# Kernel tuning notes

Hardware: AMD Instinct MI355X
Metric: run time of the kernel (lower is better)

The kernel has to match this reference:

```python
import jax, jax.numpy as jnp
import numpy as np

NEG_INF = -9e15  # matches torch reference mask value
LEAKY_SLOPE = 0.2  # alpha passed to nn.LeakyReLU


def setup_inputs() -> dict:
    key = jax.random.key(0)
    k1, k2, k3 = jax.random.split(key, 3)
    B, N, E = 256, 300, 100
    item_embeddings = jax.random.normal(k1, (B, N, E), dtype=jnp.float32)
    adj = jax.random.randint(k2, (B, N, N), 0, 5, dtype=jnp.int64)  # edge types 0..4
    A = jax.random.normal(k3, (4, E), dtype=jnp.float32)  # stacked a_0..a_3
    return {"item_embeddings": item_embeddings, "adj": adj, "A": A}


def reference(item_embeddings, adj, A):
    h = item_embeddings  # [B, N, E]
    # Original: a_input[b,i,j,:] = h[b,i,:] * h[b,j,:]; e_k = leakyrelu(a_input @ a_k).
    # Equivalent without the (B,N,N,E) tensor: e_k[b,i,j] = lrelu(sum_d h[b,i,d] h[b,j,d] A[k,d]).
    e = jnp.einsum('bid,bjd,kd->kbij', h, h, A)  # [4, B, N, N]
    e = jax.nn.leaky_relu(e, LEAKY_SLOPE)
    mask = jnp.full_like(e[0], NEG_INF)
    alpha = jnp.where(adj == 1, e[0], mask)
    alpha = jnp.where(adj == 2, e[1], alpha)
    alpha = jnp.where(adj == 3, e[2], alpha)
    alpha = jnp.where(adj == 4, e[3], alpha)
    alpha = jax.nn.softmax(alpha, axis=-1)
    return jnp.matmul(alpha, h)  # [B, N, E]
```

## Files before the change

kernel.cpp:

```cpp
#include <hip/hip_runtime.h>


typedef _Float16 half8 __attribute__((ext_vector_type(8)));
typedef _Float16 half4 __attribute__((ext_vector_type(4)));
typedef float f32x4 __attribute__((ext_vector_type(4)));

constexpr int B_ = 256, N_ = 300, E_ = 100;
constexpr float NEGINF = -9e15f;
constexpr float PADV   = -3e38f;
constexpr float LOG2E  = 1.44269504088896f;

constexpr int PART_OFF  = 69120;
constexpr int LDS_BYTES = 69120 + 11 * 7680;

#define TRD(dst, addr, off) \
  asm volatile("ds_read_b64_tr_b16 %0, %1 offset:" #off : "=v"(dst) : "v"(addr))
#define LGKM0 do { asm volatile("s_waitcnt lgkmcnt(0)" ::: "memory"); \
                   __builtin_amdgcn_sched_barrier(0); } while (0)

__global__ __launch_bounds__(768)
void gat_flash16(const float* __restrict__ H, const int* __restrict__ ADJ,
                 const float* __restrict__ A, float* __restrict__ OUT) {
  extern __shared__ char smraw[];
  _Float16* hS   = (_Float16*)smraw;
  _Float16* A16  = (_Float16*)(smraw + 68096);
  float*    part = (float*)(smraw + PART_OFF);

  const int b = blockIdx.x;
  const int tid = threadIdx.x;
  const int w = tid >> 6, lane = tid & 63;
  const int lg = lane >> 4, ll = lane & 15;

  const float* Hb  = H + (size_t)b * (N_ * E_);
  const int*   AJb = ADJ + (size_t)b * (N_ * N_);

  for (int u = tid; u < 304 * 14; u += 768) {
    const int j = u / 14, hr = u % 14;
    half8 v;
#pragma unroll
    for (int e = 0; e < 8; ++e) {
      const int d = hr * 8 + e;
      v[e] = (_Float16)((j < N_ && d < E_) ? Hb[j * E_ + d] : 0.f);
    }
    *(half8*)&hS[(((j >> 4) * 7 + (hr >> 1)) << 8) + ((j & 15) << 4) + ((hr & 1) << 3)] = v;
  }
  if (tid < 64) {
    const int k = tid >> 4, oct = tid & 15;
    half8 v;
#pragma unroll
    for (int e = 0; e < 8; ++e) {
      const int d = oct * 8 + e;
      v[e] = (_Float16)((d < E_) ? A[k * E_ + d] * LOG2E : 0.f);
    }
    *(half8*)&A16[k * 128 + oct * 8] = v;
  }
  __syncthreads();

  const unsigned ldsbase = (unsigned)(size_t)(void*)hS;
  const unsigned trlane  = (unsigned)(ll * 8 + lg * 128);

  half8 g[3][4];
  half4 gt[4];
  float m, lsum;
  f32x4 acc[7];
  const int* ajrow = AJb;

  auto prep_strip = [&](int s) {
    const int irow = s * 16 + ll;
    const int irc  = irow < N_ ? irow : N_ - 1;
    ajrow = AJb + (size_t)irc * N_;
#pragma unroll
    for (int db = 0; db < 3; ++db) {
      const int doct = db * 4 + lg;
      const half8 hi = *(const half8*)&hS[((s * 7 + (doct >> 1)) << 8) + (ll << 4) + ((doct & 1) << 3)];
#pragma unroll
      for (int k = 0; k < 4; ++k)
        g[db][k] = hi * *(const half8*)&A16[k * 128 + doct * 8];
    }
    const half4 hit = *(const half4*)&hS[((s * 7 + 6) << 8) + (ll << 4) + lg * 4];
#pragma unroll
    for (int k = 0; k < 4; ++k)
      gt[k] = hit * *(const half4*)&A16[k * 128 + 96 + lg * 4];
    m = PADV; lsum = 0.f;
#pragma unroll
    for (int t = 0; t < 7; ++t) acc[t] = (f32x4){0.f, 0.f, 0.f, 0.f};
  };

  auto load_adj = [&](int jt) -> int4 {
    int jc = jt * 16 + lg * 4;
    if (jc > N_ - 4) jc = N_ - 4;
    return *(const int4*)(ajrow + jc);
  };

  auto tile_body = [&](int jt, int4 av, bool tail) {
    f32x4 c0 = {0.f, 0.f, 0.f, 0.f}, c1 = c0, c2 = c0, c3 = c0;
#pragma unroll
    for (int db = 0; db < 3; ++db) {
      const int doct = db * 4 + lg;
      const half8 aj = *(const half8*)&hS[((jt * 7 + (doct >> 1)) << 8) + (ll << 4) + ((doct & 1) << 3)];
      c0 = __builtin_amdgcn_mfma_f32_16x16x32_f16(aj, g[db][0], c0, 0, 0, 0);
      c1 = __builtin_amdgcn_mfma_f32_16x16x32_f16(aj, g[db][1], c1, 0, 0, 0);
      c2 = __builtin_amdgcn_mfma_f32_16x16x32_f16(aj, g[db][2], c2, 0, 0, 0);
      c3 = __builtin_amdgcn_mfma_f32_16x16x32_f16(aj, g[db][3], c3, 0, 0, 0);
    }
    {
      const half4 ajt = *(const half4*)&hS[((jt * 7 + 6) << 8) + (ll << 4) + lg * 4];
      c0 = __builtin_amdgcn_mfma_f32_16x16x16f16(ajt, gt[0], c0, 0, 0, 0);
      c1 = __builtin_amdgcn_mfma_f32_16x16x16f16(ajt, gt[1], c1, 0, 0, 0);
      c2 = __builtin_amdgcn_mfma_f32_16x16x16f16(ajt, gt[2], c2, 0, 0, 0);
      c3 = __builtin_amdgcn_mfma_f32_16x16x16f16(ajt, gt[3], c3, 0, 0, 0);
    }
    const int va[4] = {av.x, av.y, av.z, av.w};
    float sv[4];
#pragma unroll
    for (int r = 0; r < 4; ++r) {
      const float e = (va[r] == 1) ? c0[r] : (va[r] == 2) ? c1[r]
                     : (va[r] == 3) ? c2[r] : c3[r];
      sv[r] = (va[r] == 0) ? NEGINF : fmaxf(e, 0.2f * e);
    }
    if (tail && lg == 3) { sv[0] = PADV; sv[1] = PADV; sv[2] = PADV; sv[3] = PADV; }

    const unsigned trb = ldsbase + (unsigned)(jt * 3584) + trlane;
    half4 tr[7];
    TRD(tr[0], trb, 0);    TRD(tr[1], trb, 512);  TRD(tr[2], trb, 1024);
    TRD(tr[3], trb, 1536); TRD(tr[4], trb, 2048); TRD(tr[5], trb, 2560);
    TRD(tr[6], trb, 3072);

    const float lmax = fmaxf(fmaxf(sv[0], sv[1]), fmaxf(sv[2], sv[3]));
    if (__any(lmax > m + 8.f)) {
      float tmax = fmaxf(lmax, __shfl_xor(lmax, 16));
      tmax = fmaxf(tmax, __shfl_xor(tmax, 32));
      const float nm = fmaxf(m, tmax);
      const float f = exp2f(m - nm);
      m = nm; lsum *= f;
#pragma unroll
      for (int t = 0; t < 7; ++t) {
        acc[t][0] *= f; acc[t][1] *= f; acc[t][2] *= f; acc[t][3] *= f;
      }
    }
    const float p0 = exp2f(sv[0] - m), p1 = exp2f(sv[1] - m);
    const float p2 = exp2f(sv[2] - m), p3 = exp2f(sv[3] - m);
    lsum += (p0 + p1) + (p2 + p3);
    half4 pb;
    pb[0] = (_Float16)p0; pb[1] = (_Float16)p1;
    pb[2] = (_Float16)p2; pb[3] = (_Float16)p3;

    LGKM0;
#pragma unroll
    for (int t = 0; t < 7; ++t)
      acc[t] = __builtin_amdgcn_mfma_f32_16x16x16f16(tr[t], pb, acc[t], 0, 0, 0);
  };

  auto store_rows = [&](int s) {
    float ls = lsum;
    ls += __shfl_xor(ls, 16);
    ls += __shfl_xor(ls, 32);
    const float rv = 1.f / ls;
    const int irow = s * 16 + ll;
    if (irow < N_) {
      float* orow = OUT + ((size_t)b * N_ + irow) * E_;
#pragma unroll
      for (int t = 0; t < 7; ++t) {
        const int e0 = t * 16 + lg * 4;
        if (e0 < E_) {
          f32x4 o = acc[t];
          o[0] *= rv; o[1] *= rv; o[2] *= rv; o[3] *= rv;
          *(f32x4*)&orow[e0] = o;
        }
      }
    }
  };

  int u = 30 * w;
  const int u1 = (w == 11) ? 361 : (u + 30);
  bool held = false;
  int s_held = 0;

  while (u < u1) {
    const int s  = u / 19;
    const int j0 = u - 19 * s;
    const int j1 = (19 < j0 + (u1 - u)) ? 19 : (j0 + (u1 - u));
    prep_strip(s);
    int4 av = load_adj(j0);
    for (int jt = j0; jt < j1; ++jt) {
      const int4 nv = (jt + 1 < j1) ? load_adj(jt + 1) : av;
      tile_body(jt, av, jt == 18);
      av = nv;
    }
    if (j0 > 0) {
      float* dst = part + (size_t)(w - 1) * 1920 + lane * 30;
#pragma unroll
      for (int t = 0; t < 7; ++t) {
        dst[4 * t + 0] = acc[t][0]; dst[4 * t + 1] = acc[t][1];
        dst[4 * t + 2] = acc[t][2]; dst[4 * t + 3] = acc[t][3];
      }
      dst[28] = m; dst[29] = lsum;
    } else if (j1 < 19) {
      held = true; s_held = s;
    } else {
      store_rows(s);
    }
    u += j1 - j0;
  }

  __syncthreads();

  if (held) {
    const float* src = part + (size_t)w * 1920 + lane * 30;
    const float mq = src[28], lq = src[29];
    const float M  = fmaxf(m, mq);
    const float f0 = exp2f(m - M), f1 = exp2f(mq - M);
    m = M;
    lsum = lsum * f0 + lq * f1;
#pragma unroll
    for (int t = 0; t < 7; ++t) {
      acc[t][0] = acc[t][0] * f0 + src[4 * t + 0] * f1;
      acc[t][1] = acc[t][1] * f0 + src[4 * t + 1] * f1;
      acc[t][2] = acc[t][2] * f0 + src[4 * t + 2] * f1;
      acc[t][3] = acc[t][3] * f0 + src[4 * t + 3] * f1;
    }
    store_rows(s_held);
  }
}

extern "C" void kernel_launch(void* const* d_in, const int* in_sizes, int n_in,
                              void* d_out, int out_size, void* d_ws, size_t ws_size,
                              hipStream_t stream) {
  const float* H  = (const float*)d_in[0];
  const int*   AJ = (const int*)d_in[1];
  const float* A  = (const float*)d_in[2];
  float* OUT = (float*)d_out;

  (void)hipFuncSetAttribute(reinterpret_cast<const void*>(gat_flash16),
                            hipFuncAttributeMaxDynamicSharedMemorySize,
                            LDS_BYTES);
  gat_flash16<<<B_, 768, LDS_BYTES, stream>>>(H, AJ, A, OUT);
}
```

Baseline: 67.73 us.

## Process key tiles in pairs per online-softmax step and rebalance wave work units

```diff
diff --git a/kernel.cpp b/kernel.cpp
--- a/kernel.cpp
+++ b/kernel.cpp
@@ -19,7 +19,7 @@
                    __builtin_amdgcn_sched_barrier(0); } while (0)
 
 __global__ __launch_bounds__(768)
-void gat_flash16(const float* __restrict__ H, const int* __restrict__ ADJ,
+void gat_flash17(const float* __restrict__ H, const int* __restrict__ ADJ,
                  const float* __restrict__ A, float* __restrict__ OUT) {
   extern __shared__ char smraw[];
   _Float16* hS   = (_Float16*)smraw;
@@ -90,6 +90,100 @@
     int jc = jt * 16 + lg * 4;
     if (jc > N_ - 4) jc = N_ - 4;
     return *(const int4*)(ajrow + jc);
+  };
+
+  auto pair_body = [&](int jtA, int4 av0, int4 av1) {
+    f32x4 c0 = {0.f, 0.f, 0.f, 0.f}, c1 = c0, c2 = c0, c3 = c0;
+#pragma unroll
+    for (int db = 0; db < 3; ++db) {
+      const int doct = db * 4 + lg;
+      const half8 aj = *(const half8*)&hS[((jtA * 7 + (doct >> 1)) << 8) + (ll << 4) + ((doct & 1) << 3)];
+      c0 = __builtin_amdgcn_mfma_f32_16x16x32_f16(aj, g[db][0], c0, 0, 0, 0);
+      c1 = __builtin_amdgcn_mfma_f32_16x16x32_f16(aj, g[db][1], c1, 0, 0, 0);
+      c2 = __builtin_amdgcn_mfma_f32_16x16x32_f16(aj, g[db][2], c2, 0, 0, 0);
+      c3 = __builtin_amdgcn_mfma_f32_16x16x32_f16(aj, g[db][3], c3, 0, 0, 0);
+    }
+    {
+      const half4 ajt = *(const half4*)&hS[((jtA * 7 + 6) << 8) + (ll << 4) + lg * 4];
+      c0 = __builtin_amdgcn_mfma_f32_16x16x16f16(ajt, gt[0], c0, 0, 0, 0);
+      c1 = __builtin_amdgcn_mfma_f32_16x16x16f16(ajt, gt[1], c1, 0, 0, 0);
+      c2 = __builtin_amdgcn_mfma_f32_16x16x16f16(ajt, gt[2], c2, 0, 0, 0);
+      c3 = __builtin_amdgcn_mfma_f32_16x16x16f16(ajt, gt[3], c3, 0, 0, 0);
+    }
+    const int vaA[4] = {av0.x, av0.y, av0.z, av0.w};
+    float svA[4];
+#pragma unroll
+    for (int r = 0; r < 4; ++r) {
+      const float e = (vaA[r] == 1) ? c0[r] : (vaA[r] == 2) ? c1[r]
+                     : (vaA[r] == 3) ? c2[r] : c3[r];
+      svA[r] = (vaA[r] == 0) ? NEGINF : fmaxf(e, 0.2f * e);
+    }
+    const int jtB = jtA + 1;
+    f32x4 d0 = {0.f, 0.f, 0.f, 0.f}, d1 = d0, d2 = d0, d3 = d0;
+#pragma unroll
+    for (int db = 0; db < 3; ++db) {
+      const int doct = db * 4 + lg;
+      const half8 aj = *(const half8*)&hS[((jtB * 7 + (doct >> 1)) << 8) + (ll << 4) + ((doct & 1) << 3)];
+      d0 = __builtin_amdgcn_mfma_f32_16x16x32_f16(aj, g[db][0], d0, 0, 0, 0);
+      d1 = __builtin_amdgcn_mfma_f32_16x16x32_f16(aj, g[db][1], d1, 0, 0, 0);
+      d2 = __builtin_amdgcn_mfma_f32_16x16x32_f16(aj, g[db][2], d2, 0, 0, 0);
+      d3 = __builtin_amdgcn_mfma_f32_16x16x32_f16(aj, g[db][3], d3, 0, 0, 0);
+    }
+    {
+      const half4 ajt = *(const half4*)&hS[((jtB * 7 + 6) << 8) + (ll << 4) + lg * 4];
+      d0 = __builtin_amdgcn_mfma_f32_16x16x16f16(ajt, gt[0], d0, 0, 0, 0);
+      d1 = __builtin_amdgcn_mfma_f32_16x16x16f16(ajt, gt[1], d1, 0, 0, 0);
+      d2 = __builtin_amdgcn_mfma_f32_16x16x16f16(ajt, gt[2], d2, 0, 0, 0);
+      d3 = __builtin_amdgcn_mfma_f32_16x16x16f16(ajt, gt[3], d3, 0, 0, 0);
+    }
+    const int vaB[4] = {av1.x, av1.y, av1.z, av1.w};
+    float svB[4];
+#pragma unroll
+    for (int r = 0; r < 4; ++r) {
+      const float e = (vaB[r] == 1) ? d0[r] : (vaB[r] == 2) ? d1[r]
+                     : (vaB[r] == 3) ? d2[r] : d3[r];
+      svB[r] = (vaB[r] == 0) ? NEGINF : fmaxf(e, 0.2f * e);
+    }
+
+    const unsigned trbA = ldsbase + (unsigned)(jtA * 3584) + trlane;
+    half4 hfA[7], hfB[7];
+    TRD(hfA[0], trbA, 0);    TRD(hfA[1], trbA, 512);  TRD(hfA[2], trbA, 1024);
+    TRD(hfA[3], trbA, 1536); TRD(hfA[4], trbA, 2048); TRD(hfA[5], trbA, 2560);
+    TRD(hfA[6], trbA, 3072);
+    TRD(hfB[0], trbA, 3584); TRD(hfB[1], trbA, 4096); TRD(hfB[2], trbA, 4608);
+    TRD(hfB[3], trbA, 5120); TRD(hfB[4], trbA, 5632); TRD(hfB[5], trbA, 6144);
+    TRD(hfB[6], trbA, 6656);
+
+    const float lmax = fmaxf(fmaxf(fmaxf(svA[0], svA[1]), fmaxf(svA[2], svA[3])),
+                             fmaxf(fmaxf(svB[0], svB[1]), fmaxf(svB[2], svB[3])));
+    if (__any(lmax > m + 8.f)) {
+      float tmax = fmaxf(lmax, __shfl_xor(lmax, 16));
+      tmax = fmaxf(tmax, __shfl_xor(tmax, 32));
+      const float nm = fmaxf(m, tmax);
+      const float f = exp2f(m - nm);
+      m = nm; lsum *= f;
+#pragma unroll
+      for (int t = 0; t < 7; ++t) {
+        acc[t][0] *= f; acc[t][1] *= f; acc[t][2] *= f; acc[t][3] *= f;
+      }
+    }
+    const float pA0 = exp2f(svA[0] - m), pA1 = exp2f(svA[1] - m);
+    const float pA2 = exp2f(svA[2] - m), pA3 = exp2f(svA[3] - m);
+    const float pB0 = exp2f(svB[0] - m), pB1 = exp2f(svB[1] - m);
+    const float pB2 = exp2f(svB[2] - m), pB3 = exp2f(svB[3] - m);
+    lsum += ((pA0 + pA1) + (pA2 + pA3)) + ((pB0 + pB1) + (pB2 + pB3));
+    half4 pbA, pbB;
+    pbA[0] = (_Float16)pA0; pbA[1] = (_Float16)pA1;
+    pbA[2] = (_Float16)pA2; pbA[3] = (_Float16)pA3;
+    pbB[0] = (_Float16)pB0; pbB[1] = (_Float16)pB1;
+    pbB[2] = (_Float16)pB2; pbB[3] = (_Float16)pB3;
+
+    LGKM0;
+#pragma unroll
+    for (int t = 0; t < 7; ++t) {
+      acc[t] = __builtin_amdgcn_mfma_f32_16x16x16f16(hfA[t], pbA, acc[t], 0, 0, 0);
+      acc[t] = __builtin_amdgcn_mfma_f32_16x16x16f16(hfB[t], pbB, acc[t], 0, 0, 0);
+    }
   };
 
   auto tile_body = [&](int jt, int4 av, bool tail) {
@@ -171,36 +265,45 @@
     }
   };
 
-  int u = 30 * w;
-  const int u1 = (w == 11) ? 361 : (u + 30);
+  int u = 16 * w;
+  const int u1 = (u + 16 < 190) ? u + 16 : 190;
   bool held = false;
   int s_held = 0;
 
   while (u < u1) {
-    const int s  = u / 19;
-    const int j0 = u - 19 * s;
-    const int j1 = (19 < j0 + (u1 - u)) ? 19 : (j0 + (u1 - u));
+    const int s  = u / 10, r0 = u - 10 * s;
+    const int r1 = (10 < r0 + (u1 - u)) ? 10 : (r0 + (u1 - u));
     prep_strip(s);
-    int4 av = load_adj(j0);
-    for (int jt = j0; jt < j1; ++jt) {
-      const int4 nv = (jt + 1 < j1) ? load_adj(jt + 1) : av;
-      tile_body(jt, av, jt == 18);
-      av = nv;
-    }
-    if (j0 > 0) {
+    int t = (r0 < 9) ? 2 * r0 : 18;
+    const int tEnd = (r1 == 10) ? 19 : ((r1 < 9) ? 2 * r1 : 18);
+
+    if (t + 1 < tEnd) {
+      int4 av0 = load_adj(t), av1 = load_adj(t + 1);
+      while (t + 1 < tEnd) {
+        const int4 nv0 = load_adj(t + 2), nv1 = load_adj(t + 3);
+        pair_body(t, av0, av1);
+        av0 = nv0; av1 = nv1;
+        t += 2;
+      }
+    }
+    if (t < tEnd) {
+      tile_body(18, load_adj(18), true);
+    }
+
+    if (r0 > 0) {
       float* dst = part + (size_t)(w - 1) * 1920 + lane * 30;
 #pragma unroll
-      for (int t = 0; t < 7; ++t) {
-        dst[4 * t + 0] = acc[t][0]; dst[4 * t + 1] = acc[t][1];
-        dst[4 * t + 2] = acc[t][2]; dst[4 * t + 3] = acc[t][3];
+      for (int tt = 0; tt < 7; ++tt) {
+        dst[4 * tt + 0] = acc[tt][0]; dst[4 * tt + 1] = acc[tt][1];
+        dst[4 * tt + 2] = acc[tt][2]; dst[4 * tt + 3] = acc[tt][3];
       }
       dst[28] = m; dst[29] = lsum;
-    } else if (j1 < 19) {
+    } else if (r1 < 10) {
       held = true; s_held = s;
     } else {
       store_rows(s);
     }
-    u += j1 - j0;
+    u += r1 - r0;
   }
 
   __syncthreads();
@@ -231,8 +334,8 @@
   const float* A  = (const float*)d_in[2];
   float* OUT = (float*)d_out;
 
-  (void)hipFuncSetAttribute(reinterpret_cast<const void*>(gat_flash16),
+  (void)hipFuncSetAttribute(reinterpret_cast<const void*>(gat_flash17),
                             hipFuncAttributeMaxDynamicSharedMemorySize,
                             LDS_BYTES);
-  gat_flash16<<<B_, 768, LDS_BYTES, stream>>>(H, AJ, A, OUT);
+  gat_flash17<<<B_, 768, LDS_BYTES, stream>>>(H, AJ, A, OUT);
 }
```

Result: slower. 73.12 us (+8.0%).
